# Kernel tuning notes

Measured on AMD Instinct MI355X. Metric: run time of the kernel, lower is better.

The kernel has to match this reference:

```python
import jax, jax.numpy as jnp
import numpy as np

N = 100000        # nodes
E = 1600000       # edges (avg degree 16)
D_IN = 128        # input feature dim
LAT = [32, 32, 32]
HID = 128
G = 1000          # graphs in batch


def _glorot(k, shape):
    lim = float(np.sqrt(6.0 / (shape[0] + shape[1])))
    return jax.random.uniform(k, shape, jnp.float32, -lim, lim)


def setup_inputs() -> dict:
    key = jax.random.key(0)
    ks = jax.random.split(key, 8)
    x = jax.random.normal(ks[0], (N, D_IN), jnp.float32)
    edge_index = jax.random.randint(ks[1], (2, E), 0, N, jnp.int32)
    # sorted graph assignment, every graph non-empty
    batch = ((jnp.arange(N, dtype=jnp.int32) * G) // N).astype(jnp.int32)
    W1 = _glorot(ks[2], (D_IN, LAT[0]));  b1 = jnp.zeros((LAT[0],), jnp.float32)
    W2 = _glorot(ks[3], (LAT[0], LAT[1])); b2 = jnp.zeros((LAT[1],), jnp.float32)
    W3 = _glorot(ks[4], (LAT[1], LAT[2])); b3 = jnp.zeros((LAT[2],), jnp.float32)
    lin1_w = _glorot(ks[5], (sum(LAT), HID)); lin1_b = jnp.zeros((HID,), jnp.float32)
    lin2_w = _glorot(ks[6], (HID, 2));        lin2_b = jnp.zeros((2,), jnp.float32)
    return dict(x=x, edge_index=edge_index, batch=batch, num_graphs=G,
                W1=W1, b1=b1, W2=W2, b2=b2, W3=W3, b3=b3,
                lin1_w=lin1_w, lin1_b=lin1_b, lin2_w=lin2_w, lin2_b=lin2_b)


def reference(x, edge_index, batch, num_graphs,
              W1, b1, W2, b2, W3, b3, lin1_w, lin1_b, lin2_w, lin2_b):
    n = x.shape[0]
    src, dst = edge_index[0], edge_index[1]
    # GCN sym-normalization with self-loops: deg[i] = 1 + in-degree(i)
    deg = jnp.ones((n,), x.dtype).at[dst].add(1.0)
    dis = jax.lax.rsqrt(deg)                      # deg^{-1/2}
    coef = (dis[src] * dis[dst])[:, None]         # [E,1] edge norm
    self_coef = (dis * dis)[:, None]              # [N,1] self-loop norm

    def gcn(h, W, b):
        h = h @ W                                  # transform first (PyG order)
        agg = jax.ops.segment_sum(h[src] * coef, dst, num_segments=n)
        return agg + h * self_coef + b

    h1 = jnp.tanh(gcn(x,  W1, b1))
    h2 = jnp.tanh(gcn(h1, W2, b2))
    h3 = jnp.tanh(gcn(h2, W3, b3))
    cat = jnp.concatenate([h1, h2, h3], axis=1)    # [N, 96]
    # readout: first node of each graph (batch is sorted)
    idx = jnp.searchsorted(batch, jnp.arange(num_graphs, dtype=batch.dtype))
    g = cat[idx]                                   # [G, 96]
    hidden = jax.nn.relu(g @ lin1_w + lin1_b)
    logits = jax.nn.log_softmax(hidden @ lin2_w + lin2_b, axis=1)
    return logits
```

## Files before the change

### kernel.cpp

```cpp
#include <hip/hip_runtime.h>
#include <math.h>


typedef int      int4v   __attribute__((ext_vector_type(4)));
typedef float    float4v __attribute__((ext_vector_type(4)));
typedef _Float16 half4v  __attribute__((ext_vector_type(4)));

#define NBLK 256
#define SB   500
#define CAPE 10240

__global__ void k_hist(const int* __restrict__ dst, int* __restrict__ blk_hist,
                       int E, int NP) {
    __shared__ int h[256];
    for (int i = threadIdx.x; i < NP; i += 256) h[i] = 0;
    __syncthreads();
    const int4v* d4 = (const int4v*)dst;
    int nv = E >> 2;
    int stride = gridDim.x * blockDim.x;
    for (int i = blockIdx.x * blockDim.x + threadIdx.x; i < nv; i += stride) {
        int4v d = __builtin_nontemporal_load(&d4[i]);
#pragma unroll
        for (int j = 0; j < 4; ++j) atomicAdd(&h[d[j] / SB], 1);
    }
    if (blockIdx.x == 0) {
        for (int e = (nv << 2) + threadIdx.x; e < E; e += blockDim.x)
            atomicAdd(&h[dst[e] / SB], 1);
    }
    __syncthreads();
    for (int i = threadIdx.x; i < NP; i += 256)
        blk_hist[blockIdx.x * NP + i] = h[i];
}

__global__ void k_total(const int* __restrict__ blk_hist, int* __restrict__ total, int NP) {
    __shared__ int s[256];
    int f = blockIdx.x;
    int acc = 0;
    for (int b = threadIdx.x; b < NBLK; b += 256) acc += blk_hist[b * NP + f];
    s[threadIdx.x] = acc;
    __syncthreads();
    for (int off = 128; off > 0; off >>= 1) {
        if (threadIdx.x < off) s[threadIdx.x] += s[threadIdx.x + off];
        __syncthreads();
    }
    if (threadIdx.x == 0) total[f] = s[0];
}

__global__ void k_sbase(const int* __restrict__ total, int* __restrict__ sbase, int NP) {
    __shared__ int s[256];
    int t = threadIdx.x;
    int v = (t < NP) ? total[t] : 0;
    s[t] = v;
    __syncthreads();
    for (int off = 1; off < 256; off <<= 1) {
        int u = (t >= off) ? s[t - off] : 0;
        __syncthreads();
        s[t] += u;
        __syncthreads();
    }
    if (t < NP) sbase[t] = s[t] - v;
    if (t == NP - 1) sbase[NP] = s[t];
}

__global__ void k_binoff(const int* __restrict__ blk_hist, const int* __restrict__ sbase,
                         int* __restrict__ blk_off, int NP) {
    __shared__ int s[NBLK];
    int f = blockIdx.x;
    int b = threadIdx.x;
    int v = blk_hist[b * NP + f];
    s[b] = v;
    __syncthreads();
    for (int off = 1; off < NBLK; off <<= 1) {
        int u = (b >= off) ? s[b - off] : 0;
        __syncthreads();
        s[b] += u;
        __syncthreads();
    }
    blk_off[b * NP + f] = sbase[f] + s[b] - v;
}

__global__ void k_split(const int* __restrict__ src, const int* __restrict__ dst,
                        const int* __restrict__ blk_off, unsigned* __restrict__ pairs,
                        int E, int NP) {
    __shared__ int goff[256];
    for (int f = threadIdx.x; f < NP; f += 256)
        goff[f] = blk_off[blockIdx.x * NP + f];
    __syncthreads();
    const int4v* d4 = (const int4v*)dst;
    const int4v* s4 = (const int4v*)src;
    int nv = E >> 2;
    int stride = gridDim.x * blockDim.x;
    for (int i = blockIdx.x * blockDim.x + threadIdx.x; i < nv; i += stride) {
        int4v d = __builtin_nontemporal_load(&d4[i]);
        int4v s = __builtin_nontemporal_load(&s4[i]);
#pragma unroll
        for (int j = 0; j < 4; ++j) {
            int f = d[j] / SB;
            int pos = atomicAdd(&goff[f], 1);
            pairs[pos] = ((unsigned)s[j] << 9) | (unsigned)(d[j] - f * SB);
        }
    }
    if (blockIdx.x == 0) {
        for (int e = (nv << 2) + threadIdx.x; e < E; e += blockDim.x) {
            int f = dst[e] / SB;
            int pos = atomicAdd(&goff[f], 1);
            pairs[pos] = ((unsigned)src[e] << 9) | (unsigned)(dst[e] - f * SB);
        }
    }
}

__global__ void __launch_bounds__(512)
k_place(const unsigned* __restrict__ pairs, const int* __restrict__ sbase,
        int* __restrict__ rowptr, float* __restrict__ dis,
        int* __restrict__ csr_src, int N, int NP) {
    __shared__ int lcnt[SB];
    __shared__ int lrp[SB + 1];
    __shared__ int sc[512];
    __shared__ int stage[CAPE];
    int f = blockIdx.x;
    int lo = f * SB;
    if (lo >= N) return;
    int hi = lo + SB; if (hi > N) hi = N;
    int sbc = hi - lo;
    int p0 = sbase[f], p1 = sbase[f + 1];
    int base = p0;
    int tid = threadIdx.x;
    for (int i = tid; i < sbc; i += 512) lcnt[i] = 0;
    __syncthreads();
    {
        int i = p0 + tid;
        for (; i + 3 * 512 < p1; i += 4 * 512) {
            unsigned a = pairs[i], c = pairs[i + 512], d = pairs[i + 1024], e = pairs[i + 1536];
            atomicAdd(&lcnt[a & 511u], 1);
            atomicAdd(&lcnt[c & 511u], 1);
            atomicAdd(&lcnt[d & 511u], 1);
            atomicAdd(&lcnt[e & 511u], 1);
        }
        for (; i < p1; i += 512) atomicAdd(&lcnt[pairs[i] & 511u], 1);
    }
    __syncthreads();
    for (int i = tid; i < sbc; i += 512) dis[lo + i] = rsqrtf(1.0f + (float)lcnt[i]);
    int v = (tid < sbc) ? lcnt[tid] : 0;
    sc[tid] = v;
    __syncthreads();
    for (int off = 1; off < 512; off <<= 1) {
        int u = (tid >= off) ? sc[tid - off] : 0;
        __syncthreads();
        sc[tid] += u;
        __syncthreads();
    }
    if (tid < sbc) lrp[tid] = sc[tid] - v;
    if (tid == 511) lrp[sbc] = sc[511];
    __syncthreads();
    int T = lrp[sbc];
    for (int i = tid; i < sbc; i += 512) rowptr[lo + i] = base + lrp[i];
    if (hi == N && tid == 0) rowptr[N] = base + T;
    for (int i = tid; i < sbc; i += 512) lcnt[i] = 0;
    __syncthreads();
    {
        int i = p0 + tid;
        for (; i + 3 * 512 < p1; i += 4 * 512) {
            unsigned pk[4] = { pairs[i], pairs[i + 512], pairs[i + 1024], pairs[i + 1536] };
#pragma unroll
            for (int j = 0; j < 4; ++j) {
                unsigned ly = pk[j] & 511u;
                int slot = lrp[ly] + atomicAdd(&lcnt[ly], 1);
                if (T <= CAPE) stage[slot] = (int)(pk[j] >> 9);
                else           csr_src[base + slot] = (int)(pk[j] >> 9);
            }
        }
        for (; i < p1; i += 512) {
            unsigned p = pairs[i];
            unsigned ly = p & 511u;
            int slot = lrp[ly] + atomicAdd(&lcnt[ly], 1);
            if (T <= CAPE) stage[slot] = (int)(p >> 9);
            else           csr_src[base + slot] = (int)(p >> 9);
        }
    }
    __syncthreads();
    if (T <= CAPE)
        for (int j = tid; j < T; j += 512) csr_src[base + j] = stage[j];
}

__global__ void k_gemm1(const float* __restrict__ h, const float* __restrict__ W,
                        const float* __restrict__ dis, _Float16* __restrict__ hps, int n) {
    __shared__ float sW[128 * 32];
    __shared__ float sh[64 * 132];
    int tid = threadIdx.x;
    int row0 = blockIdx.x * 64;
    for (int j = tid; j < 1024; j += 128)
        *(float4*)&sW[j * 4] = *(const float4*)&W[j * 4];
    for (int j = tid; j < 2048; j += 128) {
        int r = j >> 5, c4 = j & 31;
        float4v v = {0.f, 0.f, 0.f, 0.f};
        if (row0 + r < n)
            v = __builtin_nontemporal_load((const float4v*)&h[(size_t)(row0 + r) * 128 + c4 * 4]);
        *(float4v*)&sh[r * 132 + c4 * 4] = v;
    }
    __syncthreads();
    int rg = tid >> 3;
    int cg = tid & 7;
    float acc[4][4] = {};
    const float* shp = &sh[(rg * 4) * 132];
    const float* swp = &sW[cg * 4];
#pragma unroll 8
    for (int k4 = 0; k4 < 32; ++k4) {
        float4 hv[4], wv[4];
#pragma unroll
        for (int r = 0; r < 4; ++r) hv[r] = *(const float4*)&shp[r * 132 + k4 * 4];
#pragma unroll
        for (int t = 0; t < 4; ++t) wv[t] = *(const float4*)&swp[(k4 * 4 + t) * 32];
#pragma unroll
        for (int r = 0; r < 4; ++r) {
            const float hr[4] = {hv[r].x, hv[r].y, hv[r].z, hv[r].w};
#pragma unroll
            for (int t = 0; t < 4; ++t) {
                acc[r][0] += hr[t] * wv[t].x;
                acc[r][1] += hr[t] * wv[t].y;
                acc[r][2] += hr[t] * wv[t].z;
                acc[r][3] += hr[t] * wv[t].w;
            }
        }
    }
#pragma unroll
    for (int r = 0; r < 4; ++r) {
        int row = row0 + rg * 4 + r;
        if (row < n) {
            float dv = dis[row];
            half4v o = { (_Float16)(acc[r][0] * dv), (_Float16)(acc[r][1] * dv),
                         (_Float16)(acc[r][2] * dv), (_Float16)(acc[r][3] * dv) };
            *(half4v*)&hps[(size_t)row * 32 + cg * 4] = o;
        }
    }
}

template <bool FUSE>
__global__ void k_agg(const _Float16* __restrict__ hps, const int* __restrict__ rowptr,
                      const int* __restrict__ csr_src, const float* __restrict__ dis,
                      const float* __restrict__ bias, float* __restrict__ outc,
                      int n, const float* __restrict__ Wn, _Float16* __restrict__ hpsn) {
    __shared__ float sW[32 * 32];
    if (FUSE) {
        for (int i = threadIdx.x; i < 1024; i += 256) sW[i] = Wn[i];
        __syncthreads();
    }
    int g    = (blockIdx.x * blockDim.x + threadIdx.x) >> 5;
    int lane = threadIdx.x & 31;
    if (g >= n) return;
    float acc = (float)hps[(size_t)g * 32 + lane];
    int e0 = rowptr[g], e1 = rowptr[g + 1];
    int e = e0;
    while (e < e1) {
        int m = e1 - e; if (m > 32) m = 32;
        int sv = (e + lane < e1) ? __builtin_nontemporal_load(&csr_src[e + lane]) : 0;
        int k = 0;
        for (; k + 16 <= m; k += 16) {
            float v[16];
#pragma unroll
            for (int j = 0; j < 16; ++j) {
                int s = __shfl(sv, k + j, 32);
                v[j] = (float)hps[(size_t)s * 32 + lane];
            }
            float a = ((v[0] + v[1]) + (v[2] + v[3])) + ((v[4] + v[5]) + (v[6] + v[7]));
            float b = ((v[8] + v[9]) + (v[10] + v[11])) + ((v[12] + v[13]) + (v[14] + v[15]));
            acc += a + b;
        }
        for (; k + 8 <= m; k += 8) {
            float v[8];
#pragma unroll
            for (int j = 0; j < 8; ++j) {
                int s = __shfl(sv, k + j, 32);
                v[j] = (float)hps[(size_t)s * 32 + lane];
            }
            acc += ((v[0] + v[1]) + (v[2] + v[3])) + ((v[4] + v[5]) + (v[6] + v[7]));
        }
        if (k + 4 <= m) {
            float v[4];
#pragma unroll
            for (int j = 0; j < 4; ++j) {
                int s = __shfl(sv, k + j, 32);
                v[j] = (float)hps[(size_t)s * 32 + lane];
            }
            acc += (v[0] + v[1]) + (v[2] + v[3]);
            k += 4;
        }
        for (; k < m; ++k) {
            int s = __shfl(sv, k, 32);
            acc += (float)hps[(size_t)s * 32 + lane];
        }
        e += m;
    }
    float dg = dis[g];
    float v = tanhf(dg * acc + bias[lane]);
    __builtin_nontemporal_store(v, &outc[(size_t)g * 96 + lane]);
    if (FUSE) {
        float a2 = 0.0f;
#pragma unroll
        for (int k = 0; k < 32; ++k)
            a2 += __shfl(v, k, 32) * sW[k * 32 + lane];
        hpsn[(size_t)g * 32 + lane] = (_Float16)(dg * a2);
    }
}

__global__ void k_idx(const int* __restrict__ batch, int* __restrict__ idx, int n, int g) {
    int i = blockIdx.x * blockDim.x + threadIdx.x;
    if (i >= g) return;
    int lo = 0, hi = n;
    while (lo < hi) {
        int mid = (lo + hi) >> 1;
        if (batch[mid] < i) lo = mid + 1; else hi = mid;
    }
    idx[i] = lo;
}

__global__ void k_head(const float* __restrict__ cat, const int* __restrict__ idx,
                       const float* __restrict__ w1, const float* __restrict__ b1,
                       const float* __restrict__ w2, const float* __restrict__ b2,
                       float* __restrict__ out) {
    __shared__ float gv[96];
    __shared__ float s0[128];
    __shared__ float s1[128];
    int g = blockIdx.x, t = threadIdx.x;
    int node = idx[g];
    if (t < 96) gv[t] = cat[(size_t)node * 96 + t];
    __syncthreads();
    float acc = b1[t];
#pragma unroll 8
    for (int i = 0; i < 96; ++i) acc += gv[i] * w1[i * 128 + t];
    float h = fmaxf(acc, 0.0f);
    s0[t] = h * w2[t * 2 + 0];
    s1[t] = h * w2[t * 2 + 1];
    __syncthreads();
    for (int off = 64; off > 0; off >>= 1) {
        if (t < off) { s0[t] += s0[t + off]; s1[t] += s1[t + off]; }
        __syncthreads();
    }
    if (t == 0) {
        float l0 = s0[0] + b2[0];
        float l1 = s1[0] + b2[1];
        float m  = fmaxf(l0, l1);
        float lse = m + logf(expf(l0 - m) + expf(l1 - m));
        out[(size_t)g * 2 + 0] = l0 - lse;
        out[(size_t)g * 2 + 1] = l1 - lse;
    }
}

extern "C" void kernel_launch(void* const* d_in, const int* in_sizes, int n_in,
                              void* d_out, int out_size, void* d_ws, size_t ws_size,
                              hipStream_t stream) {
    const float* x    = (const float*)d_in[0];
    const int*   ei   = (const int*)d_in[1];
    const int*   batch= (const int*)d_in[2];
    const float* W1   = (const float*)d_in[4];
    const float* b1   = (const float*)d_in[5];
    const float* W2   = (const float*)d_in[6];
    const float* b2   = (const float*)d_in[7];
    const float* W3   = (const float*)d_in[8];
    const float* b3   = (const float*)d_in[9];
    const float* l1w  = (const float*)d_in[10];
    const float* l1b  = (const float*)d_in[11];
    const float* l2w  = (const float*)d_in[12];
    const float* l2b  = (const float*)d_in[13];
    float* out = (float*)d_out;

    const int N = in_sizes[0] / 128;
    const int E = in_sizes[1] / 2;
    const int G = out_size / 2;
    const int* src = ei;
    const int* dst = ei + E;

    const int NP = (N + SB - 1) / SB;

    char* w = (char*)d_ws;
    auto alloc = [&](size_t bytes) {
        char* p = w;
        w += (bytes + 255) & ~(size_t)255;
        return p;
    };
    float*    dis      = (float*)   alloc((size_t)N * 4);
    int*      rowptr   = (int*)     alloc((size_t)(N + 1) * 4);
    int*      csr_src  = (int*)     alloc((size_t)E * 4);
    int*      blk_hist = (int*)     alloc((size_t)NBLK * NP * 4);
    int*      total    = (int*)     alloc((size_t)NP * 4);
    int*      sbase    = (int*)     alloc((size_t)(NP + 1) * 4);
    int*      blk_off  = (int*)     alloc((size_t)NBLK * NP * 4);
    unsigned* pairs    = (unsigned*)alloc((size_t)E * 4);
    _Float16* hpsA     = (_Float16*)alloc((size_t)N * 32 * 2);
    _Float16* hpsB     = (_Float16*)alloc((size_t)N * 32 * 2);
    float*    catb     = (float*)   alloc((size_t)N * 96 * 4);
    int*      idx      = (int*)     alloc((size_t)G * 4);

    const int nodes_bl = (N * 32 + 255) / 256;
    const int gemm_bl  = (N + 63) / 64;

    k_hist  <<<NBLK, 256, 0, stream>>>(dst, blk_hist, E, NP);
    k_total <<<NP,   256, 0, stream>>>(blk_hist, total, NP);
    k_sbase <<<1,    256, 0, stream>>>(total, sbase, NP);
    k_binoff<<<NP,  NBLK, 0, stream>>>(blk_hist, sbase, blk_off, NP);
    k_split <<<NBLK, 256, 0, stream>>>(src, dst, blk_off, pairs, E, NP);
    k_place <<<NP,   512, 0, stream>>>(pairs, sbase, rowptr, dis, csr_src, N, NP);

    k_gemm1<<<gemm_bl, 128, 0, stream>>>(x, W1, dis, hpsA, N);
    k_agg<true ><<<nodes_bl, 256, 0, stream>>>(hpsA, rowptr, csr_src, dis, b1, catb + 0,  N, W2, hpsB);
    k_agg<true ><<<nodes_bl, 256, 0, stream>>>(hpsB, rowptr, csr_src, dis, b2, catb + 32, N, W3, hpsA);
    k_agg<false><<<nodes_bl, 256, 0, stream>>>(hpsA, rowptr, csr_src, dis, b3, catb + 64, N, nullptr, nullptr);

    k_idx<<<(G + 255) / 256, 256, 0, stream>>>(batch, idx, N, G);
    k_head<<<G, 128, 0, stream>>>(catb, idx, l1w, l1b, l2w, l2b, out);
}
```

Measured before the change: 228.9 us.

## Split GCN feature aggregation into two 16-column halves with separate GEMM kernels

Each 32-wide fp16 feature table is split into two 16-column tables, each 3.2 MB instead of 6.4 MB, so each aggregation pass gathers from a smaller working set that fits cache better. Aggregation now runs twice per layer with 16-lane groups. The layer-2 and layer-3 transforms are no longer fused into the aggregation epilogue; a templated GEMM kernel reads them back from the fp32 concat buffer. This trades more kernel launches, extra passes over the CSR index arrays and an extra read of activations for better gather locality.

After: 382.9 us. 67.3% more time.

```diff
diff --git a/kernel.cpp b/kernel.cpp
--- a/kernel.cpp
+++ b/kernel.cpp
@@ -182,32 +182,35 @@
         for (int j = tid; j < T; j += 512) csr_src[base + j] = stage[j];
 }
 
-__global__ void k_gemm1(const float* __restrict__ h, const float* __restrict__ W,
-                        const float* __restrict__ dis, _Float16* __restrict__ hps, int n) {
-    __shared__ float sW[128 * 32];
-    __shared__ float sh[64 * 132];
+template <int K>
+__global__ void k_gemmK(const float* __restrict__ h, int ldh, const float* __restrict__ W,
+                        const float* __restrict__ dis, _Float16* __restrict__ hA,
+                        _Float16* __restrict__ hB, int n) {
+    __shared__ float sW[K * 32];
+    __shared__ float sh[64 * (K + 4)];
+    const int KP = K + 4;
     int tid = threadIdx.x;
     int row0 = blockIdx.x * 64;
-    for (int j = tid; j < 1024; j += 128)
+    for (int j = tid; j < K * 8; j += 128)
         *(float4*)&sW[j * 4] = *(const float4*)&W[j * 4];
-    for (int j = tid; j < 2048; j += 128) {
-        int r = j >> 5, c4 = j & 31;
+    for (int j = tid; j < 16 * K; j += 128) {
+        int r = j / (K / 4), c4 = j % (K / 4);
         float4v v = {0.f, 0.f, 0.f, 0.f};
         if (row0 + r < n)
-            v = __builtin_nontemporal_load((const float4v*)&h[(size_t)(row0 + r) * 128 + c4 * 4]);
-        *(float4v*)&sh[r * 132 + c4 * 4] = v;
+            v = __builtin_nontemporal_load((const float4v*)&h[(size_t)(row0 + r) * ldh + c4 * 4]);
+        *(float4v*)&sh[r * KP + c4 * 4] = v;
     }
     __syncthreads();
     int rg = tid >> 3;
     int cg = tid & 7;
     float acc[4][4] = {};
-    const float* shp = &sh[(rg * 4) * 132];
+    const float* shp = &sh[(rg * 4) * KP];
     const float* swp = &sW[cg * 4];
 #pragma unroll 8
-    for (int k4 = 0; k4 < 32; ++k4) {
+    for (int k4 = 0; k4 < K / 4; ++k4) {
         float4 hv[4], wv[4];
 #pragma unroll
-        for (int r = 0; r < 4; ++r) hv[r] = *(const float4*)&shp[r * 132 + k4 * 4];
+        for (int r = 0; r < 4; ++r) hv[r] = *(const float4*)&shp[r * KP + k4 * 4];
 #pragma unroll
         for (int t = 0; t < 4; ++t) wv[t] = *(const float4*)&swp[(k4 * 4 + t) * 32];
 #pragma unroll
@@ -229,37 +232,31 @@
             float dv = dis[row];
             half4v o = { (_Float16)(acc[r][0] * dv), (_Float16)(acc[r][1] * dv),
                          (_Float16)(acc[r][2] * dv), (_Float16)(acc[r][3] * dv) };
-            *(half4v*)&hps[(size_t)row * 32 + cg * 4] = o;
-        }
-    }
-}
-
-template <bool FUSE>
-__global__ void k_agg(const _Float16* __restrict__ hps, const int* __restrict__ rowptr,
-                      const int* __restrict__ csr_src, const float* __restrict__ dis,
-                      const float* __restrict__ bias, float* __restrict__ outc,
-                      int n, const float* __restrict__ Wn, _Float16* __restrict__ hpsn) {
-    __shared__ float sW[32 * 32];
-    if (FUSE) {
-        for (int i = threadIdx.x; i < 1024; i += 256) sW[i] = Wn[i];
-        __syncthreads();
-    }
-    int g    = (blockIdx.x * blockDim.x + threadIdx.x) >> 5;
-    int lane = threadIdx.x & 31;
+            if (cg < 4) *(half4v*)&hA[(size_t)row * 16 + cg * 4] = o;
+            else        *(half4v*)&hB[(size_t)row * 16 + (cg - 4) * 4] = o;
+        }
+    }
+}
+
+__global__ void k_agg16(const _Float16* __restrict__ hp, const int* __restrict__ rowptr,
+                        const int* __restrict__ csr_src, const float* __restrict__ dis,
+                        const float* __restrict__ bias, float* __restrict__ outc, int n) {
+    int g    = (blockIdx.x * blockDim.x + threadIdx.x) >> 4;
+    int lane = threadIdx.x & 15;
     if (g >= n) return;
-    float acc = (float)hps[(size_t)g * 32 + lane];
+    float acc = (float)hp[(size_t)g * 16 + lane];
     int e0 = rowptr[g], e1 = rowptr[g + 1];
     int e = e0;
     while (e < e1) {
-        int m = e1 - e; if (m > 32) m = 32;
+        int m = e1 - e; if (m > 16) m = 16;
         int sv = (e + lane < e1) ? __builtin_nontemporal_load(&csr_src[e + lane]) : 0;
         int k = 0;
         for (; k + 16 <= m; k += 16) {
             float v[16];
 #pragma unroll
             for (int j = 0; j < 16; ++j) {
-                int s = __shfl(sv, k + j, 32);
-                v[j] = (float)hps[(size_t)s * 32 + lane];
+                int s = __shfl(sv, k + j, 16);
+                v[j] = (float)hp[(size_t)s * 16 + lane];
             }
             float a = ((v[0] + v[1]) + (v[2] + v[3])) + ((v[4] + v[5]) + (v[6] + v[7]));
             float b = ((v[8] + v[9]) + (v[10] + v[11])) + ((v[12] + v[13]) + (v[14] + v[15]));
@@ -269,8 +266,8 @@
             float v[8];
 #pragma unroll
             for (int j = 0; j < 8; ++j) {
-                int s = __shfl(sv, k + j, 32);
-                v[j] = (float)hps[(size_t)s * 32 + lane];
+                int s = __shfl(sv, k + j, 16);
+                v[j] = (float)hp[(size_t)s * 16 + lane];
             }
             acc += ((v[0] + v[1]) + (v[2] + v[3])) + ((v[4] + v[5]) + (v[6] + v[7]));
         }
@@ -278,28 +275,20 @@
             float v[4];
 #pragma unroll
             for (int j = 0; j < 4; ++j) {
-                int s = __shfl(sv, k + j, 32);
-                v[j] = (float)hps[(size_t)s * 32 + lane];
+                int s = __shfl(sv, k + j, 16);
+                v[j] = (float)hp[(size_t)s * 16 + lane];
             }
             acc += (v[0] + v[1]) + (v[2] + v[3]);
             k += 4;
         }
         for (; k < m; ++k) {
-            int s = __shfl(sv, k, 32);
-            acc += (float)hps[(size_t)s * 32 + lane];
+            int s = __shfl(sv, k, 16);
+            acc += (float)hp[(size_t)s * 16 + lane];
         }
         e += m;
     }
-    float dg = dis[g];
-    float v = tanhf(dg * acc + bias[lane]);
+    float v = tanhf(dis[g] * acc + bias[lane]);
     __builtin_nontemporal_store(v, &outc[(size_t)g * 96 + lane]);
-    if (FUSE) {
-        float a2 = 0.0f;
-#pragma unroll
-        for (int k = 0; k < 32; ++k)
-            a2 += __shfl(v, k, 32) * sW[k * 32 + lane];
-        hpsn[(size_t)g * 32 + lane] = (_Float16)(dg * a2);
-    }
 }
 
 __global__ void k_idx(const int* __restrict__ batch, int* __restrict__ idx, int n, int g) {
@@ -385,13 +374,15 @@
     int*      sbase    = (int*)     alloc((size_t)(NP + 1) * 4);
     int*      blk_off  = (int*)     alloc((size_t)NBLK * NP * 4);
     unsigned* pairs    = (unsigned*)alloc((size_t)E * 4);
-    _Float16* hpsA     = (_Float16*)alloc((size_t)N * 32 * 2);
-    _Float16* hpsB     = (_Float16*)alloc((size_t)N * 32 * 2);
+    _Float16* hA0      = (_Float16*)alloc((size_t)N * 16 * 2);
+    _Float16* hB0      = (_Float16*)alloc((size_t)N * 16 * 2);
+    _Float16* hA1      = (_Float16*)alloc((size_t)N * 16 * 2);
+    _Float16* hB1      = (_Float16*)alloc((size_t)N * 16 * 2);
     float*    catb     = (float*)   alloc((size_t)N * 96 * 4);
     int*      idx      = (int*)     alloc((size_t)G * 4);
 
-    const int nodes_bl = (N * 32 + 255) / 256;
-    const int gemm_bl  = (N + 63) / 64;
+    const int nodes16_bl = (N * 16 + 255) / 256;
+    const int gemm_bl    = (N + 63) / 64;
 
     k_hist  <<<NBLK, 256, 0, stream>>>(dst, blk_hist, E, NP);
     k_total <<<NP,   256, 0, stream>>>(blk_hist, total, NP);
@@ -400,10 +391,15 @@
     k_split <<<NBLK, 256, 0, stream>>>(src, dst, blk_off, pairs, E, NP);
     k_place <<<NP,   512, 0, stream>>>(pairs, sbase, rowptr, dis, csr_src, N, NP);
 
-    k_gemm1<<<gemm_bl, 128, 0, stream>>>(x, W1, dis, hpsA, N);
-    k_agg<true ><<<nodes_bl, 256, 0, stream>>>(hpsA, rowptr, csr_src, dis, b1, catb + 0,  N, W2, hpsB);
-    k_agg<true ><<<nodes_bl, 256, 0, stream>>>(hpsB, rowptr, csr_src, dis, b2, catb + 32, N, W3, hpsA);
-    k_agg<false><<<nodes_bl, 256, 0, stream>>>(hpsA, rowptr, csr_src, dis, b3, catb + 64, N, nullptr, nullptr);
+    k_gemmK<128><<<gemm_bl, 128, 0, stream>>>(x, 128, W1, dis, hA0, hB0, N);
+    k_agg16<<<nodes16_bl, 256, 0, stream>>>(hA0, rowptr, csr_src, dis, b1 + 0,  catb + 0,  N);
+    k_agg16<<<nodes16_bl, 256, 0, stream>>>(hB0, rowptr, csr_src, dis, b1 + 16, catb + 16, N);
+    k_gemmK<32><<<gemm_bl, 128, 0, stream>>>(catb + 0, 96, W2, dis, hA1, hB1, N);
+    k_agg16<<<nodes16_bl, 256, 0, stream>>>(hA1, rowptr, csr_src, dis, b2 + 0,  catb + 32, N);
+    k_agg16<<<nodes16_bl, 256, 0, stream>>>(hB1, rowptr, csr_src, dis, b2 + 16, catb + 48, N);
+    k_gemmK<32><<<gemm_bl, 128, 0, stream>>>(catb + 32, 96, W3, dis, hA0, hB0, N);
+    k_agg16<<<nodes16_bl, 256, 0, stream>>>(hA0, rowptr, csr_src, dis, b3 + 0,  catb + 64, N);
+    k_agg16<<<nodes16_bl, 256, 0, stream>>>(hB0, rowptr, csr_src, dis, b3 + 16, catb + 80, N);
 
     k_idx<<<(G + 255) / 256, 256, 0, stream>>>(batch, idx, N, G);
     k_head<<<G, 128, 0, stream>>>(catb, idx, l1w, l1b, l2w, l2b, out);
```
